# Optimization experiments

Hardware: AMD Instinct MI355X
Metric: run time of the kernel (lower is better)

## Reference

```python
import jax, jax.numpy as jnp
import numpy as np

N_NODES = 100000
N_EDGES = 1600000
IN_CH, HID_CH, OUT_CH = 64, 64, 16
N_REL = 8


def setup_inputs() -> dict:
    key = jax.random.key(0)
    ks = jax.random.split(key, 10)
    x = jax.random.normal(ks[0], (N_NODES, IN_CH), dtype=jnp.float32)
    edge_index = jax.random.randint(ks[1], (2, N_EDGES), 0, N_NODES, dtype=jnp.int64)
    edge_type = jax.random.randint(ks[2], (N_EDGES,), 0, N_REL, dtype=jnp.int64)
    # RGCNConv params: per-relation weight, root weight, bias (Glorot-ish scale)
    def glorot(k, shape):
        fan = shape[-2] + shape[-1]
        return jax.random.normal(k, shape, dtype=jnp.float32) * jnp.sqrt(2.0 / fan)
    W1 = glorot(ks[3], (N_REL, IN_CH, HID_CH))
    root1 = glorot(ks[4], (IN_CH, HID_CH))
    b1 = jnp.zeros((HID_CH,), dtype=jnp.float32)
    W2 = glorot(ks[5], (N_REL, HID_CH, OUT_CH))
    root2 = glorot(ks[6], (HID_CH, OUT_CH))
    b2 = jnp.zeros((OUT_CH,), dtype=jnp.float32)
    return {"x": x, "edge_index": edge_index, "edge_type": edge_type,
            "W1": W1, "root1": root1, "b1": b1,
            "W2": W2, "root2": root2, "b2": b2}


def rgcn_conv(x, src, dst, edge_type, W_rel, W_root, bias):
    """PyG RGCNConv: out_i = x_i @ W_root + b + sum_r mean_{j in N_r(i)} x_j @ W_r.
    Mean is linear, so aggregate raw features per relation, then transform."""
    n = x.shape[0]
    xs = x[src]  # [E, F] gathered source features (hot memory-bound op)
    out = x @ W_root + bias
    for r in range(W_rel.shape[0]):  # small fixed relation count
        mask = (edge_type == r).astype(x.dtype)  # [E]
        agg = jax.ops.segment_sum(xs * mask[:, None], dst, num_segments=n)  # [N, F]
        cnt = jax.ops.segment_sum(mask, dst, num_segments=n)  # [N]
        agg = agg / jnp.clip(cnt, 1.0)[:, None]  # mean aggr; 0 when no edges
        out = out + agg @ W_rel[r]
    return out


def reference(x, edge_index, edge_type, W1, root1, b1, W2, root2, b2):
    src, dst = edge_index[0], edge_index[1]
    h = rgcn_conv(x, src, dst, edge_type, W1, root1, b1)
    h = jax.nn.relu(h)
    h = rgcn_conv(h, src, dst, edge_type, W2, root2, b2)
    # global_mean_pool with a single graph: mean over nodes -> [1, out]
    g = jnp.mean(h, axis=0, keepdims=True)
    return jax.nn.log_softmax(g, axis=1)
```

## Files before the change

kernel.cpp:

```cpp
#include <hip/hip_runtime.h>
#include <hip/hip_bf16.h>


#define CH 64
#define BK_EDGES 2048
#define CAP 12288
#define KB 128

typedef __attribute__((ext_vector_type(8))) short short8;
typedef __attribute__((ext_vector_type(4))) float f32x4;

__device__ inline ushort f2bf(float f) {
    unsigned b = __float_as_uint(f);
    unsigned r = (b + 0x7FFFu + ((b >> 16) & 1u)) >> 16;
    return (ushort)r;
}
__device__ inline float bf2f(ushort u) {
    return __uint_as_float(((unsigned)u) << 16);
}


__global__ __launch_bounds__(256) void prep_kernel(
    const int* __restrict__ src, const int* __restrict__ dst,
    const int* __restrict__ etype, const float* __restrict__ x,
    const float* __restrict__ W1, const float* __restrict__ root1,
    int* __restrict__ gBucketCnt, int2* __restrict__ bucket_buf,
    ushort* __restrict__ xbf, ushort* __restrict__ wf,
    int E, int N, int nBin, int nXbf)
{
    __shared__ int s_k[BK_EDGES];
    __shared__ int s_y[BK_EDGES];
    __shared__ int hist[256], scanv[256], lcur[256], bstart[256], gbase[256];
    const int t = threadIdx.x;
    const int bid = blockIdx.x;

    if (bid >= nBin) {
        if (bid < nBin + nXbf) {
            int i = (bid - nBin) * 256 + t;
            if (i < N * CH / 4) {
                float4 v = ((const float4*)x)[i];
                ((ushort4*)xbf)[i] = make_ushort4(f2bf(v.x), f2bf(v.y), f2bf(v.z), f2bf(v.w));
            }
        } else {
            int idx = (bid - nBin - nXbf) * 256 + t;
            if (idx < 9 * 2 * 4 * 64 * 8) {
                int j    = idx & 7;
                int lane = (idx >> 3) & 63;
                int ct   = (idx >> 9) & 3;
                int ks   = (idx >> 11) & 1;
                int rel  = idx >> 12;
                int k = ks * 32 + (lane >> 4) * 8 + j;
                int n = ct * 16 + (lane & 15);
                float v = (rel < 8) ? W1[((size_t)rel * 64 + k) * 64 + n]
                                    : root1[(size_t)k * 64 + n];
                wf[idx] = f2bf(v);
            }
        }
        return;
    }

    const int e0 = bid * BK_EDGES;
    const int cnt = min(BK_EDGES, E - e0);

    hist[t] = 0;
    __syncthreads();

    int myb[8], myk[8], myy[8];
    #pragma unroll
    for (int i = 0; i < 8; ++i) {
        int li = t + i * 256;
        if (li < cnt) {
            int e = e0 + li;
            int r = etype[e];
            int k = r * N + dst[e];
            myk[i] = k;
            myy[i] = (r << 17) | src[e];
            myb[i] = k >> 12;
            atomicAdd(&hist[myb[i]], 1);
        } else myb[i] = -1;
    }
    __syncthreads();

    int v = hist[t];
    scanv[t] = v;
    __syncthreads();
    for (int off = 1; off < 256; off <<= 1) {
        int u = (t >= off) ? scanv[t - off] : 0;
        __syncthreads();
        scanv[t] += u;
        __syncthreads();
    }
    int excl = scanv[t] - v;
    bstart[t] = excl;
    lcur[t] = excl;
    __syncthreads();

    #pragma unroll
    for (int i = 0; i < 8; ++i) {
        if (myb[i] >= 0) {
            int p = atomicAdd(&lcur[myb[i]], 1);
            s_k[p] = myk[i];
            s_y[p] = myy[i];
        }
    }
    __syncthreads();

    if (v > 0) gbase[t] = atomicAdd(&gBucketCnt[t], v);
    __syncthreads();

    for (int p = t; p < cnt; p += 256) {
        int k = s_k[p];
        int b = k >> 12;
        int gp = gbase[b] + (p - bstart[b]);
        if (gp < CAP)
            bucket_buf[(size_t)b * CAP + gp] = make_int2(k, s_y[p]);
    }
}


__global__ __launch_bounds__(1024) void build_kernel(
    const int2* __restrict__ bucket_buf, const int* __restrict__ gBucketCnt,
    int* __restrict__ rowptr, float* __restrict__ inv,
    int* __restrict__ perm, int N)
{
    __shared__ int hist[4096];
    __shared__ int cur[4096];
    __shared__ int part[1024];
    const int b = blockIdx.x;
    const int t = threadIdx.x;
    const int nb = min(gBucketCnt[b], CAP);
    const int2* rec = bucket_buf + (size_t)b * CAP;

    int bc = (t < 256) ? gBucketCnt[t] : 0;
    part[t] = bc;
    __syncthreads();
    for (int off = 1; off < 1024; off <<= 1) {
        int u = (t >= off) ? part[t - off] : 0;
        __syncthreads();
        part[t] += u;
        __syncthreads();
    }
    __shared__ int baseS;
    if (t == b) baseS = part[t] - bc;
    __syncthreads();
    const int base = baseS;

    for (int i = t; i < 4096; i += 1024) hist[i] = 0;
    __syncthreads();
    for (int j = t; j < nb; j += 1024) atomicAdd(&hist[rec[j].x & 4095], 1);
    __syncthreads();

    const int i0 = t * 4;
    int h0 = hist[i0], h1 = hist[i0 + 1], h2 = hist[i0 + 2], h3 = hist[i0 + 3];
    int s = h0 + h1 + h2 + h3;
    part[t] = s;
    __syncthreads();
    for (int off = 1; off < 1024; off <<= 1) {
        int u = (t >= off) ? part[t - off] : 0;
        __syncthreads();
        part[t] += u;
        __syncthreads();
    }
    int run = base + part[t] - s;
    int hk[4] = {h0, h1, h2, h3};
    #pragma unroll
    for (int k = 0; k < 4; ++k) {
        cur[i0 + k] = run;
        rowptr[b * 4096 + i0 + k] = run;
        inv[b * 4096 + i0 + k] = 1.0f / (float)max(hk[k], 1);
        run += hk[k];
    }
    __syncthreads();

    for (int j = t; j < nb; j += 1024) {
        int k = rec[j].x, y = rec[j].y;
        int lk = k & 4095;
        int pos = atomicAdd(&cur[lk], 1);
        perm[pos] = y & 0x1FFFF;
    }
}


__global__ __launch_bounds__(256) void rgcn1_fused_kernel(
    const int* __restrict__ rowptr, const int* __restrict__ perm,
    const float* __restrict__ inv, const ushort* __restrict__ xbf,
    const ushort* __restrict__ wfrag, const float* __restrict__ b1,
    const int* __restrict__ srcE, const int* __restrict__ dstE,
    const int* __restrict__ etypeE, float* __restrict__ kappa,
    float* __restrict__ h, int N, int E)
{
    if (blockIdx.x < KB) {
        const int chunk = (E + KB - 1) / KB;
        const int lo = blockIdx.x * chunk;
        const int hi = min(lo + chunk, E);
        for (int e = lo + (int)threadIdx.x; e < hi; e += 256) {
            int r = etypeE[e];
            int d = dstE[e];
            int s = srcE[e];
            unsafeAtomicAdd(&kappa[(s << 3) | r], inv[(size_t)r * N + d]);
        }
        return;
    }

    __shared__ ushort Abuf[4][16 * 72];
    __shared__ int    rpS[4][144];
    __shared__ float  invS[4][128];
    const int widx = threadIdx.x >> 6;
    const int lane = threadIdx.x & 63;
    const int wid = ((blockIdx.x - KB) << 2) | widx;
    const int base = wid << 4;
    if (base >= N) return;

    const int m0 = lane & 15;
    const int q  = lane >> 4;
    const int sg = lane >> 3;
    const int cg = lane & 7;
    ushort* ab = Abuf[widx];
    int*    rpL = rpS[widx];
    float*  ivL = invS[widx];

    for (int i = lane; i < 136; i += 64) {
        int r = i / 17, mm = i - r * 17;
        rpL[i] = rowptr[(size_t)r * N + base + mm];
    }
    for (int i = lane; i < 128; i += 64)
        ivL[i] = inv[(size_t)(i >> 4) * N + base + (i & 15)];

    f32x4 acc4[4];
    #pragma unroll
    for (int ct = 0; ct < 4; ++ct) acc4[ct] = (f32x4)(0.0f);

    for (int r = 0; r < 8; ++r) {
        const int iA = r * 17 + sg;
        const int iB = iA + 8;
        int jA = rpL[iA], eA = rpL[iA + 1];
        int jB = rpL[iB], eB = rpL[iB + 1];
        float a[8] = {}, bacc[8] = {};
        int s0A = perm[(jA     < eA) ? jA     : 0];
        int s1A = perm[(jA + 1 < eA) ? jA + 1 : 0];
        int s0B = perm[(jB     < eB) ? jB     : 0];
        int s1B = perm[(jB + 1 < eB) ? jB + 1 : 0];
        while (jA < eA || jB < eB) {
            short8 r0A = *(const short8*)&xbf[(size_t)s0A * CH + (cg << 3)];
            short8 r1A = *(const short8*)&xbf[(size_t)s1A * CH + (cg << 3)];
            short8 r0B = *(const short8*)&xbf[(size_t)s0B * CH + (cg << 3)];
            short8 r1B = *(const short8*)&xbf[(size_t)s1B * CH + (cg << 3)];
            int t0A = perm[(jA + 2 < eA) ? jA + 2 : 0];
            int t1A = perm[(jA + 3 < eA) ? jA + 3 : 0];
            int t0B = perm[(jB + 2 < eB) ? jB + 2 : 0];
            int t1B = perm[(jB + 3 < eB) ? jB + 3 : 0];
            float m0A = (jA     < eA) ? 1.f : 0.f;
            float m1A = (jA + 1 < eA) ? 1.f : 0.f;
            float m0B = (jB     < eB) ? 1.f : 0.f;
            float m1B = (jB + 1 < eB) ? 1.f : 0.f;
            #pragma unroll
            for (int k = 0; k < 8; ++k) {
                a[k]    += m0A * bf2f((ushort)r0A[k]) + m1A * bf2f((ushort)r1A[k]);
                bacc[k] += m0B * bf2f((ushort)r0B[k]) + m1B * bf2f((ushort)r1B[k]);
            }
            s0A = t0A; s1A = t1A; s0B = t0B; s1B = t1B;
            jA += 2; jB += 2;
        }
        const float ivA = ivL[(r << 4) | sg];
        const float ivB = ivL[(r << 4) | (8 + sg)];
        short8 oA, oB;
        #pragma unroll
        for (int k = 0; k < 8; ++k) {
            oA[k] = (short)f2bf(a[k] * ivA);
            oB[k] = (short)f2bf(bacc[k] * ivB);
        }
        *(short8*)&ab[sg * 72 + (cg << 3)]       = oA;
        *(short8*)&ab[(8 + sg) * 72 + (cg << 3)] = oB;

        #pragma unroll
        for (int s = 0; s < 2; ++s) {
            short8 av = *(short8*)&ab[m0 * 72 + s * 32 + q * 8];
            #pragma unroll
            for (int ct = 0; ct < 4; ++ct) {
                short8 bv = *(const short8*)&wfrag[(((size_t)(r * 2 + s) * 4 + ct) * 64 + lane) * 8];
                acc4[ct] = __builtin_amdgcn_mfma_f32_16x16x32_bf16(av, bv, acc4[ct], 0, 0, 0);
            }
        }
    }

    {
        int node = min(base + m0, N - 1);
        #pragma unroll
        for (int s = 0; s < 2; ++s) {
            short8 av = *(const short8*)&xbf[(size_t)node * CH + s * 32 + q * 8];
            #pragma unroll
            for (int ct = 0; ct < 4; ++ct) {
                short8 bv = *(const short8*)&wfrag[(((size_t)(8 * 2 + s) * 4 + ct) * 64 + lane) * 8];
                acc4[ct] = __builtin_amdgcn_mfma_f32_16x16x32_bf16(av, bv, acc4[ct], 0, 0, 0);
            }
        }
    }

    #pragma unroll
    for (int ct = 0; ct < 4; ++ct) {
        int c = ct * 16 + m0;
        float bb = b1[c];
        #pragma unroll
        for (int v = 0; v < 4; ++v) {
            int node = base + q * 4 + v;
            if (node < N)
                h[(size_t)node * CH + c] = fmaxf(acc4[ct][v] + bb, 0.f);
        }
    }
}


__global__ __launch_bounds__(256) void kred_kernel(
    const float* __restrict__ h, const float* __restrict__ kappa,
    float* __restrict__ sacc, int N)
{
    const int lane = threadIdx.x & 63;
    const int w = threadIdx.x >> 6;
    int wave = (blockIdx.x << 2) | w;
    const int wstride = gridDim.x << 2;
    float racc[9] = {};
    for (int i = wave; i < N; i += wstride) {
        float hv = h[(size_t)i * CH + lane];
        #pragma unroll
        for (int r = 0; r < 8; ++r) racc[r] += hv * kappa[i * 8 + r];
        racc[8] += hv;
    }
    __shared__ float red[4][9][64];
    #pragma unroll
    for (int r = 0; r < 9; ++r) red[w][r][lane] = racc[r];
    __syncthreads();
    if (w == 0) {
        #pragma unroll
        for (int r = 0; r < 9; ++r) {
            float s4 = red[0][r][lane] + red[1][r][lane] + red[2][r][lane] + red[3][r][lane];
            unsafeAtomicAdd(&sacc[r * 64 + lane], s4);
        }
    }
}

__global__ void finalize_kernel(const float* __restrict__ sacc, const float* __restrict__ root2,
                                const float* __restrict__ W2, const float* __restrict__ b2,
                                float* __restrict__ out, float invN)
{
    __shared__ float g[16];
    int t = threadIdx.x;
    if (t < 16) {
        const float* s0 = sacc + 512;
        float acc = 0.f;
        for (int c = 0; c < 64; ++c) acc += s0[c] * root2[c * 16 + t];
        for (int r = 0; r < 8; ++r) {
            const float* sr = sacc + r * 64;
            for (int c = 0; c < 64; ++c) acc += sr[c] * W2[(r * 64 + c) * 16 + t];
        }
        g[t] = acc * invN + b2[t];
    }
    __syncthreads();
    if (t < 16) {
        float m = -1e30f;
        for (int i = 0; i < 16; ++i) m = fmaxf(m, g[i]);
        float s = 0.f;
        for (int i = 0; i < 16; ++i) s += expf(g[i] - m);
        out[t] = g[t] - (m + logf(s));
    }
}


extern "C" void kernel_launch(void* const* d_in, const int* in_sizes, int n_in,
                              void* d_out, int out_size, void* d_ws, size_t ws_size,
                              hipStream_t stream)
{
    const float* x     = (const float*)d_in[0];
    const int*   eidx  = (const int*)d_in[1];
    const int*   etype = (const int*)d_in[2];
    const float* W1    = (const float*)d_in[3];
    const float* root1 = (const float*)d_in[4];
    const float* b1    = (const float*)d_in[5];
    const float* W2    = (const float*)d_in[6];
    const float* root2 = (const float*)d_in[7];
    const float* b2    = (const float*)d_in[8];
    float* out = (float*)d_out;

    const int E = in_sizes[1] / 2;
    const int N = in_sizes[0] / CH;
    const int NKEY = N * 8;
    const int NBUK = (NKEY + 4095) / 4096;
    const int KSPACE = NBUK << 12;
    const int* srcI = eidx;
    const int* dstI = eidx + E;

    int* wsi = (int*)d_ws;
    int*   gBucketCnt = wsi;
    float* sacc       = (float*)(gBucketCnt + 256);
    float* kappa      = sacc + 576;
    float* inv        = kappa + NKEY;
    int*   rowptr     = (int*)(inv + KSPACE);
    int*   perm       = rowptr + KSPACE + 16;
    size_t off = (size_t)((perm + E) - wsi);
    off = (off + 1) & ~(size_t)1;
    int2*  bucket_buf = (int2*)(wsi + off);
    off += (size_t)NBUK * CAP * 2;
    off = (off + 7) & ~(size_t)7;
    ushort* xbf = (ushort*)(wsi + off);
    ushort* wfg = xbf + (size_t)N * CH;
    float*  h   = (float*)(wfg + 36864);

    hipMemsetAsync(d_ws, 0, (size_t)(256 + 576 + NKEY) * 4, stream);

    const int nBin = (E + BK_EDGES - 1) / BK_EDGES;
    const int nXbf = (N * CH / 4 + 255) / 256;
    const int nWf  = (36864 + 255) / 256;
    prep_kernel<<<nBin + nXbf + nWf, 256, 0, stream>>>(
        srcI, dstI, etype, x, W1, root1, gBucketCnt, bucket_buf, xbf, wfg,
        E, N, nBin, nXbf);

    build_kernel<<<NBUK, 1024, 0, stream>>>(
        bucket_buf, gBucketCnt, rowptr, inv, perm, N);

    const int tiles = (N + 15) / 16;
    rgcn1_fused_kernel<<<KB + (tiles + 3) / 4, 256, 0, stream>>>(
        rowptr, perm, inv, xbf, wfg, b1, srcI, dstI, etype, kappa, h, N, E);

    kred_kernel<<<1024, 256, 0, stream>>>(h, kappa, sacc, N);
    finalize_kernel<<<1, 64, 0, stream>>>(sacc, root2, W2, b2, out, 1.0f / (float)N);
}
```

Before: 295.7 us.

## Gather neighbor features as fp8 and add nontemporal loads in layer-one kernel

Prep now also writes an fp8 copy of x, and the layer-one neighbor gather reads 8 bytes per lane instead of 16, unpacking with the hardware fp8-to-f32 conversion. The goal is to halve gather traffic in the memory-bound aggregation. The kappa atomic pass gets more blocks and a 4-way unrolled loop, and several streaming loads and stores become nontemporal. The cost is precision: features drop to fp8 before averaging, which may exceed tolerance, and prep does extra conversion and writes.

```diff
diff --git a/kernel.cpp b/kernel.cpp
--- a/kernel.cpp
+++ b/kernel.cpp
@@ -5,10 +5,11 @@
 #define CH 64
 #define BK_EDGES 2048
 #define CAP 12288
-#define KB 128
+#define KB 256
 
 typedef __attribute__((ext_vector_type(8))) short short8;
 typedef __attribute__((ext_vector_type(4))) float f32x4;
+typedef __attribute__((ext_vector_type(2))) float f32x2;
 
 __device__ inline ushort f2bf(float f) {
     unsigned b = __float_as_uint(f);
@@ -17,6 +18,14 @@
 }
 __device__ inline float bf2f(ushort u) {
     return __uint_as_float(((unsigned)u) << 16);
+}
+
+__device__ inline void acc8fp8(float* a, uint2 w, float m) {
+    f32x2 p;
+    p = __builtin_amdgcn_cvt_pk_f32_fp8(w.x, 0); a[0] += m * p.x; a[1] += m * p.y;
+    p = __builtin_amdgcn_cvt_pk_f32_fp8(w.x, 1); a[2] += m * p.x; a[3] += m * p.y;
+    p = __builtin_amdgcn_cvt_pk_f32_fp8(w.y, 0); a[4] += m * p.x; a[5] += m * p.y;
+    p = __builtin_amdgcn_cvt_pk_f32_fp8(w.y, 1); a[6] += m * p.x; a[7] += m * p.y;
 }
 
 
@@ -25,7 +34,8 @@
     const int* __restrict__ etype, const float* __restrict__ x,
     const float* __restrict__ W1, const float* __restrict__ root1,
     int* __restrict__ gBucketCnt, int2* __restrict__ bucket_buf,
-    ushort* __restrict__ xbf, ushort* __restrict__ wf,
+    ushort* __restrict__ xbf, unsigned char* __restrict__ xq,
+    ushort* __restrict__ wf,
     int E, int N, int nBin, int nXbf)
 {
     __shared__ int s_k[BK_EDGES];
@@ -40,6 +50,9 @@
             if (i < N * CH / 4) {
                 float4 v = ((const float4*)x)[i];
                 ((ushort4*)xbf)[i] = make_ushort4(f2bf(v.x), f2bf(v.y), f2bf(v.z), f2bf(v.w));
+                int p8 = __builtin_amdgcn_cvt_pk_fp8_f32(v.x, v.y, 0, 0);
+                p8 = __builtin_amdgcn_cvt_pk_fp8_f32(v.z, v.w, p8, 1);
+                ((unsigned int*)xq)[i] = (unsigned int)p8;
             }
         } else {
             int idx = (bid - nBin - nXbf) * 256 + t;
@@ -184,6 +197,7 @@
 __global__ __launch_bounds__(256) void rgcn1_fused_kernel(
     const int* __restrict__ rowptr, const int* __restrict__ perm,
     const float* __restrict__ inv, const ushort* __restrict__ xbf,
+    const unsigned char* __restrict__ xq,
     const ushort* __restrict__ wfrag, const float* __restrict__ b1,
     const int* __restrict__ srcE, const int* __restrict__ dstE,
     const int* __restrict__ etypeE, float* __restrict__ kappa,
@@ -193,7 +207,30 @@
         const int chunk = (E + KB - 1) / KB;
         const int lo = blockIdx.x * chunk;
         const int hi = min(lo + chunk, E);
-        for (int e = lo + (int)threadIdx.x; e < hi; e += 256) {
+        int e = lo + (int)threadIdx.x;
+        for (; e + 768 < hi; e += 1024) {
+            int r0 = __builtin_nontemporal_load(etypeE + e);
+            int r1 = __builtin_nontemporal_load(etypeE + e + 256);
+            int r2 = __builtin_nontemporal_load(etypeE + e + 512);
+            int r3 = __builtin_nontemporal_load(etypeE + e + 768);
+            int d0 = __builtin_nontemporal_load(dstE + e);
+            int d1 = __builtin_nontemporal_load(dstE + e + 256);
+            int d2 = __builtin_nontemporal_load(dstE + e + 512);
+            int d3 = __builtin_nontemporal_load(dstE + e + 768);
+            int s0 = __builtin_nontemporal_load(srcE + e);
+            int s1 = __builtin_nontemporal_load(srcE + e + 256);
+            int s2 = __builtin_nontemporal_load(srcE + e + 512);
+            int s3 = __builtin_nontemporal_load(srcE + e + 768);
+            float i0 = inv[(size_t)r0 * N + d0];
+            float i1 = inv[(size_t)r1 * N + d1];
+            float i2 = inv[(size_t)r2 * N + d2];
+            float i3 = inv[(size_t)r3 * N + d3];
+            unsafeAtomicAdd(&kappa[(s0 << 3) | r0], i0);
+            unsafeAtomicAdd(&kappa[(s1 << 3) | r1], i1);
+            unsafeAtomicAdd(&kappa[(s2 << 3) | r2], i2);
+            unsafeAtomicAdd(&kappa[(s3 << 3) | r3], i3);
+        }
+        for (; e < hi; e += 256) {
             int r = etypeE[e];
             int d = dstE[e];
             int s = srcE[e];
@@ -221,10 +258,10 @@
 
     for (int i = lane; i < 136; i += 64) {
         int r = i / 17, mm = i - r * 17;
-        rpL[i] = rowptr[(size_t)r * N + base + mm];
+        rpL[i] = __builtin_nontemporal_load(rowptr + (size_t)r * N + base + mm);
     }
     for (int i = lane; i < 128; i += 64)
-        ivL[i] = inv[(size_t)(i >> 4) * N + base + (i & 15)];
+        ivL[i] = __builtin_nontemporal_load(inv + (size_t)(i >> 4) * N + base + (i & 15));
 
     f32x4 acc4[4];
     #pragma unroll
@@ -236,28 +273,27 @@
         int jA = rpL[iA], eA = rpL[iA + 1];
         int jB = rpL[iB], eB = rpL[iB + 1];
         float a[8] = {}, bacc[8] = {};
-        int s0A = perm[(jA     < eA) ? jA     : 0];
-        int s1A = perm[(jA + 1 < eA) ? jA + 1 : 0];
-        int s0B = perm[(jB     < eB) ? jB     : 0];
-        int s1B = perm[(jB + 1 < eB) ? jB + 1 : 0];
+        int s0A = __builtin_nontemporal_load(perm + ((jA     < eA) ? jA     : 0));
+        int s1A = __builtin_nontemporal_load(perm + ((jA + 1 < eA) ? jA + 1 : 0));
+        int s0B = __builtin_nontemporal_load(perm + ((jB     < eB) ? jB     : 0));
+        int s1B = __builtin_nontemporal_load(perm + ((jB + 1 < eB) ? jB + 1 : 0));
         while (jA < eA || jB < eB) {
-            short8 r0A = *(const short8*)&xbf[(size_t)s0A * CH + (cg << 3)];
-            short8 r1A = *(const short8*)&xbf[(size_t)s1A * CH + (cg << 3)];
-            short8 r0B = *(const short8*)&xbf[(size_t)s0B * CH + (cg << 3)];
-            short8 r1B = *(const short8*)&xbf[(size_t)s1B * CH + (cg << 3)];
-            int t0A = perm[(jA + 2 < eA) ? jA + 2 : 0];
-            int t1A = perm[(jA + 3 < eA) ? jA + 3 : 0];
-            int t0B = perm[(jB + 2 < eB) ? jB + 2 : 0];
-            int t1B = perm[(jB + 3 < eB) ? jB + 3 : 0];
+            uint2 w0A = *(const uint2*)(xq + (size_t)s0A * CH + (cg << 3));
+            uint2 w1A = *(const uint2*)(xq + (size_t)s1A * CH + (cg << 3));
+            uint2 w0B = *(const uint2*)(xq + (size_t)s0B * CH + (cg << 3));
+            uint2 w1B = *(const uint2*)(xq + (size_t)s1B * CH + (cg << 3));
+            int t0A = __builtin_nontemporal_load(perm + ((jA + 2 < eA) ? jA + 2 : 0));
+            int t1A = __builtin_nontemporal_load(perm + ((jA + 3 < eA) ? jA + 3 : 0));
+            int t0B = __builtin_nontemporal_load(perm + ((jB + 2 < eB) ? jB + 2 : 0));
+            int t1B = __builtin_nontemporal_load(perm + ((jB + 3 < eB) ? jB + 3 : 0));
             float m0A = (jA     < eA) ? 1.f : 0.f;
             float m1A = (jA + 1 < eA) ? 1.f : 0.f;
             float m0B = (jB     < eB) ? 1.f : 0.f;
             float m1B = (jB + 1 < eB) ? 1.f : 0.f;
-            #pragma unroll
-            for (int k = 0; k < 8; ++k) {
-                a[k]    += m0A * bf2f((ushort)r0A[k]) + m1A * bf2f((ushort)r1A[k]);
-                bacc[k] += m0B * bf2f((ushort)r0B[k]) + m1B * bf2f((ushort)r1B[k]);
-            }
+            acc8fp8(a,    w0A, m0A);
+            acc8fp8(a,    w1A, m1A);
+            acc8fp8(bacc, w0B, m0B);
+            acc8fp8(bacc, w1B, m1B);
             s0A = t0A; s1A = t1A; s0B = t0B; s1B = t1B;
             jA += 2; jB += 2;
         }
@@ -287,7 +323,8 @@
         int node = min(base + m0, N - 1);
         #pragma unroll
         for (int s = 0; s < 2; ++s) {
-            short8 av = *(const short8*)&xbf[(size_t)node * CH + s * 32 + q * 8];
+            short8 av = __builtin_nontemporal_load(
+                (const short8*)&xbf[(size_t)node * CH + s * 32 + q * 8]);
             #pragma unroll
             for (int ct = 0; ct < 4; ++ct) {
                 short8 bv = *(const short8*)&wfrag[(((size_t)(8 * 2 + s) * 4 + ct) * 64 + lane) * 8];
@@ -304,7 +341,8 @@
         for (int v = 0; v < 4; ++v) {
             int node = base + q * 4 + v;
             if (node < N)
-                h[(size_t)node * CH + c] = fmaxf(acc4[ct][v] + bb, 0.f);
+                __builtin_nontemporal_store(fmaxf(acc4[ct][v] + bb, 0.f),
+                                            &h[(size_t)node * CH + c]);
         }
     }
 }
@@ -320,7 +358,7 @@
     const int wstride = gridDim.x << 2;
     float racc[9] = {};
     for (int i = wave; i < N; i += wstride) {
-        float hv = h[(size_t)i * CH + lane];
+        float hv = __builtin_nontemporal_load(&h[(size_t)i * CH + lane]);
         #pragma unroll
         for (int r = 0; r < 8; ++r) racc[r] += hv * kappa[i * 8 + r];
         racc[8] += hv;
@@ -402,7 +440,8 @@
     off = (off + 7) & ~(size_t)7;
     ushort* xbf = (ushort*)(wsi + off);
     ushort* wfg = xbf + (size_t)N * CH;
-    float*  h   = (float*)(wfg + 36864);
+    unsigned char* xq = (unsigned char*)(wfg + 36864);
+    float*  h   = (float*)(xq + (size_t)N * CH);
 
     hipMemsetAsync(d_ws, 0, (size_t)(256 + 576 + NKEY) * 4, stream);
 
@@ -410,7 +449,7 @@
     const int nXbf = (N * CH / 4 + 255) / 256;
     const int nWf  = (36864 + 255) / 256;
     prep_kernel<<<nBin + nXbf + nWf, 256, 0, stream>>>(
-        srcI, dstI, etype, x, W1, root1, gBucketCnt, bucket_buf, xbf, wfg,
+        srcI, dstI, etype, x, W1, root1, gBucketCnt, bucket_buf, xbf, xq, wfg,
         E, N, nBin, nXbf);
 
     build_kernel<<<NBUK, 1024, 0, stream>>>(
@@ -418,7 +457,7 @@
 
     const int tiles = (N + 15) / 16;
     rgcn1_fused_kernel<<<KB + (tiles + 3) / 4, 256, 0, stream>>>(
-        rowptr, perm, inv, xbf, wfg, b1, srcI, dstI, etype, kappa, h, N, E);
+        rowptr, perm, inv, xbf, xq, wfg, b1, srcI, dstI, etype, kappa, h, N, E);
 
     kred_kernel<<<1024, 256, 0, stream>>>(h, kappa, sacc, N);
     finalize_kernel<<<1, 64, 0, stream>>>(sacc, root2, W2, b2, out, 1.0f / (float)N);
```

After: 351.5 us. 1.19x slower.
